# Kernel tuning notes

Hardware: AMD Instinct MI355X
Metric: run time of the kernel (lower is better)

## Reference

```python
import jax, jax.numpy as jnp
import numpy as np

X_DIM, Z_DIM, H, B, T = 257, 16, 128, 256, 512


def _p(key, shape, scale=0.05):
    return jax.random.normal(key, shape, jnp.float32) * scale


def setup_inputs() -> dict:
    key = jax.random.key(0)
    ks = jax.random.split(key, 16)
    z4 = jnp.zeros((4 * H,), jnp.float32)
    return {
        "x": jax.random.uniform(ks[0], (B, X_DIM, T), jnp.float32),
        "eps": jax.random.normal(ks[1], (T, B, Z_DIM), jnp.float32),
        # rnn_g_x: backward LSTM over x
        "Wih_gx": _p(ks[2], (4 * H, X_DIM)), "Whh_gx": _p(ks[3], (4 * H, H)),
        "bih_gx": z4, "bhh_gx": z4,
        # rnn_g_z: forward LSTM cell over sampled z
        "Wih_gz": _p(ks[4], (4 * H, Z_DIM)), "Whh_gz": _p(ks[5], (4 * H, H)),
        "bih_gz": z4, "bhh_gz": z4,
        # mlp_inference (one dense layer, tanh) + heads
        "W0": _p(ks[6], (H, 2 * H)), "b0": jnp.zeros((H,), jnp.float32),
        "Wm": _p(ks[7], (Z_DIM, H)), "bm": jnp.zeros((Z_DIM,), jnp.float32),
        "Wv": _p(ks[8], (Z_DIM, H)), "bv": jnp.zeros((Z_DIM,), jnp.float32),
        # decoder rnn_h + gen_logvar
        "Wih_h": _p(ks[9], (4 * H, Z_DIM)), "Whh_h": _p(ks[10], (4 * H, H)),
        "bih_h": z4, "bhh_h": z4,
        "Wy": _p(ks[11], (X_DIM, H)), "by": jnp.zeros((X_DIM,), jnp.float32),
    }


def _lstm(xs, Wih, Whh, b, reverse=False):
    # xs: (T, B, in); single-layer LSTM, PyTorch gate order i,f,g,o
    Bn, Hd = xs.shape[1], Whh.shape[1]

    def step(carry, x_t):
        h, c = carry
        g = x_t @ Wih.T + h @ Whh.T + b
        i, f, gg, o = jnp.split(g, 4, axis=-1)
        c = jax.nn.sigmoid(f) * c + jax.nn.sigmoid(i) * jnp.tanh(gg)
        h = jax.nn.sigmoid(o) * jnp.tanh(c)
        return (h, c), h

    init = (jnp.zeros((Bn, Hd), xs.dtype), jnp.zeros((Bn, Hd), xs.dtype))
    _, hs = jax.lax.scan(step, init, xs, reverse=reverse)
    return hs


def reference(x, eps, Wih_gx, Whh_gx, bih_gx, bhh_gx,
              Wih_gz, Whh_gz, bih_gz, bhh_gz,
              W0, b0, Wm, bm, Wv, bv,
              Wih_h, Whh_h, bih_h, bhh_h, Wy, by):
    xt = jnp.transpose(x, (2, 0, 1))  # (T, B, x_dim)
    # g_x = flip(LSTM(flip(x))) == backward-direction LSTM
    g_x = _lstm(xt, Wih_gx, Whh_gx, bih_gx + bhh_gx, reverse=True)
    bz = bih_gz + bhh_gz
    Hz = Whh_gz.shape[1]

    def inf_step(carry, inp):
        g_z, c_z = carry  # hidden of rnn_g_z BEFORE seeing current z
        gx_t, eps_t = inp
        h = jnp.tanh(jnp.concatenate([gx_t, g_z], axis=-1) @ W0.T + b0)
        mean = h @ Wm.T + bm
        logvar = h @ Wv.T + bv
        z_t = eps_t * jnp.exp(0.5 * logvar) + mean  # reparameterize
        # one LSTM-cell step of rnn_g_z on z_t (used at next timestep)
        g = z_t @ Wih_gz.T + g_z @ Whh_gz.T + bz
        i, f, gg, o = jnp.split(g, 4, axis=-1)
        c_z = jax.nn.sigmoid(f) * c_z + jax.nn.sigmoid(i) * jnp.tanh(gg)
        g_z = jax.nn.sigmoid(o) * jnp.tanh(c_z)
        return (g_z, c_z), (mean, logvar, z_t)

    Bn = xt.shape[1]
    init = (jnp.zeros((Bn, Hz), x.dtype), jnp.zeros((Bn, Hz), x.dtype))
    _, (mean, logvar, z) = jax.lax.scan(inf_step, init, (g_x, eps))
    # generation
    hdec = _lstm(z, Wih_h, Whh_h, bih_h + bhh_h)
    y = jnp.exp(hdec @ Wy.T + by)  # (T, B, x_dim)
    perm = lambda a: jnp.transpose(a, (1, 2, 0))  # -> (B, dim, T)
    return perm(y), perm(mean), perm(logvar), perm(z)
```

## Files before the change

kernel.cpp:

```cpp
#include <hip/hip_runtime.h>
#include <stdint.h>

#define T_SEQ 512
#define BATCH 256
#define HID   128
#define G4    512
#define XD    257
#define ZD    16

__device__ __forceinline__ float bf2f(uint16_t u) {
  union { uint32_t i; float f; } v; v.i = ((uint32_t)u) << 16; return v.f;
}
__device__ __forceinline__ uint16_t f2bf(float f) {
  union { float f; uint32_t i; } v; v.f = f;
  uint32_t r = v.i + 0x7fffu + ((v.i >> 16) & 1u);
  return (uint16_t)(r >> 16);
}
__device__ __forceinline__ float sigf(float x) { return 1.0f / (1.0f + __expf(-x)); }
__device__ __forceinline__ float tanhfast(float x) { return 2.0f / (1.0f + __expf(-2.0f * x)) - 1.0f; }
__device__ __forceinline__ float gate_act(float pre, bool isg) {
  float s = isg ? (-2.0f * pre) : (-pre);
  float r = 1.0f / (1.0f + __expf(s));
  return isg ? (2.0f * r - 1.0f) : r;
}

__global__ void k_prep(const float* __restrict__ Wih_gx, const float* __restrict__ Wy,
                       float* __restrict__ wT, float* __restrict__ wyT) {
  int idx = blockIdx.x * 256 + threadIdx.x;
  const int N1 = XD * G4;
  const int N2 = HID * XD;
  if (idx < N1) {
    int j = idx & (G4 - 1), d = idx >> 9;
    wT[idx] = Wih_gx[j * XD + d];
  } else if (idx < N1 + N2) {
    int i2 = idx - N1;
    int u = i2 / XD, d = i2 % XD;
    wyT[i2] = Wy[d * HID + u];
  }
}

__global__ __launch_bounds__(256) void k_proj(
    const float* __restrict__ x, const float* __restrict__ wT,
    const float* __restrict__ bih, const float* __restrict__ bhh,
    uint16_t* __restrict__ px) {
  __shared__ uint16_t xs[XD * 66];
  int tid = threadIdx.x;
  int t0 = blockIdx.x * 64, b = blockIdx.y;
  int lane = tid & 63;
  {
    int t = tid & 63, d0 = tid >> 6;
    for (int d = d0; d < XD; d += 4)
      xs[d * 66 + t] = f2bf(x[((size_t)b * XD + d) * T_SEQ + t0 + t]);
  }
  __syncthreads();
  int w = __builtin_amdgcn_readfirstlane(tid >> 6);
  for (int p = 0; p < 8; ++p) {
    int j0 = w * 128 + p * 16;
    float acc[16];
#pragma unroll
    for (int i = 0; i < 16; ++i) acc[i] = bih[j0 + i] + bhh[j0 + i];
    for (int d = 0; d < XD; ++d) {
      float xv = bf2f(xs[d * 66 + lane]);
      const float* wrow = wT + (size_t)d * G4 + j0;
#pragma unroll
      for (int i = 0; i < 16; ++i) acc[i] = fmaf(wrow[i], xv, acc[i]);
    }
    size_t base = ((size_t)(t0 + lane) * BATCH + b) * G4 + j0;
    uint32_t pk[8];
#pragma unroll
    for (int i = 0; i < 8; ++i)
      pk[i] = (uint32_t)f2bf(acc[2 * i]) | ((uint32_t)f2bf(acc[2 * i + 1]) << 16);
    uint4* dst = (uint4*)(px + base);
    dst[0] = make_uint4(pk[0], pk[1], pk[2], pk[3]);
    dst[1] = make_uint4(pk[4], pk[5], pk[6], pk[7]);
  }
}

__global__ __launch_bounds__(512, 2) void k_lstm_gx(
    const uint16_t* __restrict__ px, const float* __restrict__ Whh,
    uint16_t* __restrict__ gx) {
  __shared__ __align__(16) float hl[2][HID];
  int tid = threadIdx.x, b = blockIdx.x;
  int u = tid >> 2, g = tid & 3;
  int j = g * HID + u;
  float wr[HID];
#pragma unroll
  for (int k = 0; k < HID; ++k) wr[k] = Whh[(size_t)j * HID + k];
  if (tid < HID) hl[0][tid] = 0.0f;
  float c = 0.0f;
  int cur = 0;
  int ql = (tid & 63) & ~3;
  bool isg = (g == 2);
  uint16_t pcur = px[((size_t)(T_SEQ - 1) * BATCH + b) * G4 + j];
  __syncthreads();
  for (int t = T_SEQ - 1; t >= 0; --t) {
    int tn = t > 0 ? t - 1 : 0;
    uint16_t pnext = px[((size_t)tn * BATCH + b) * G4 + j];
    float pre = bf2f(pcur);
    const float4* h4 = (const float4*)hl[cur];
#pragma unroll
    for (int k4 = 0; k4 < HID / 4; ++k4) {
      float4 h = h4[k4];
      pre = fmaf(wr[4 * k4 + 0], h.x, pre);
      pre = fmaf(wr[4 * k4 + 1], h.y, pre);
      pre = fmaf(wr[4 * k4 + 2], h.z, pre);
      pre = fmaf(wr[4 * k4 + 3], h.w, pre);
    }
    float act = gate_act(pre, isg);
    float af = __shfl(act, ql + 1);
    float ag = __shfl(act, ql + 2);
    float ao = __shfl(act, ql + 3);
    if (g == 0) {
      c = af * c + act * ag;
      float h = ao * tanhfast(c);
      hl[cur ^ 1][u] = h;
      gx[((size_t)t * BATCH + b) * HID + u] = f2bf(h);
    }
    cur ^= 1;
    pcur = pnext;
    __syncthreads();
  }
}

__global__ __launch_bounds__(512, 2) void k_inf(
    const uint16_t* __restrict__ gx, const float* __restrict__ eps,
    const float* __restrict__ Wih_gz, const float* __restrict__ Whh_gz,
    const float* __restrict__ bih_gz, const float* __restrict__ bhh_gz,
    const float* __restrict__ W0, const float* __restrict__ b0,
    const float* __restrict__ Wm, const float* __restrict__ bm,
    const float* __restrict__ Wv, const float* __restrict__ bv,
    float* __restrict__ zbuf, float* __restrict__ out_mean,
    float* __restrict__ out_logvar, float* __restrict__ out_z) {
  __shared__ float wgzT2[ZD * 512];
  __shared__ __align__(16) float gxl[HID];
  __shared__ __align__(16) float gzl[2][HID];
  __shared__ __align__(16) float hvec[HID];
  __shared__ __align__(16) float zl[ZD];
  int tid = threadIdx.x, b = blockIdx.x;
  int u = tid >> 2, g = tid & 3;
  int j = g * HID + u;
#pragma unroll
  for (int k = 0; k < ZD; ++k) wgzT2[k * 512 + tid] = Wih_gz[(size_t)j * ZD + k];
  float wzr[HID];
#pragma unroll
  for (int k = 0; k < HID; ++k) wzr[k] = Whh_gz[(size_t)j * HID + k];
  float bzr = bih_gz[j] + bhh_gz[j];
  float w0r[64];
#pragma unroll
  for (int i = 0; i < 64; ++i) w0r[i] = W0[(size_t)u * 256 + g * 64 + i];
  float b0r = b0[u];
  int o = tid >> 5, lo = tid & 31;
  float wmr[8];
  {
    const float* Wsel = (lo < 16) ? (Wm + (size_t)o * HID + lo * 8)
                                  : (Wv + (size_t)o * HID + (lo - 16) * 8);
#pragma unroll
    for (int i = 0; i < 8; ++i) wmr[i] = Wsel[i];
  }
  float bmr = bm[o], bvr = bv[o];
  float czr = 0.0f;
  int cur = 0;
  int ql = (tid & 63) & ~3;
  bool isg = (g == 2);
  if (tid < HID) {
    gzl[0][tid] = 0.0f;
    gxl[tid] = bf2f(gx[(size_t)b * HID + tid]);
  }
  float epcur = (lo == 0) ? eps[(size_t)b * ZD + o] : 0.0f;
  __syncthreads();
  for (int t = 0; t < T_SEQ; ++t) {
    int tn = (t < T_SEQ - 1) ? t + 1 : t;
    float gxnext = (tid < HID) ? bf2f(gx[((size_t)tn * BATCH + b) * HID + tid]) : 0.0f;
    float epnext = (lo == 0) ? eps[((size_t)tn * BATCH + b) * ZD + o] : 0.0f;
    {
      const float4* src = (const float4*)((g < 2) ? (gxl + g * 64) : (gzl[cur] + (g - 2) * 64));
      float p = 0.0f;
#pragma unroll
      for (int i4 = 0; i4 < 16; ++i4) {
        float4 v = src[i4];
        p = fmaf(w0r[4 * i4 + 0], v.x, p);
        p = fmaf(w0r[4 * i4 + 1], v.y, p);
        p = fmaf(w0r[4 * i4 + 2], v.z, p);
        p = fmaf(w0r[4 * i4 + 3], v.w, p);
      }
      p += __shfl_xor(p, 1);
      p += __shfl_xor(p, 2);
      if (g == 0) hvec[u] = tanhfast(p + b0r);
    }
    __syncthreads();
    {
      int hbase = (lo & 15) * 8;
      const float4* hh = (const float4*)(hvec + hbase);
      float4 h0 = hh[0], h1 = hh[1];
      float p = wmr[0] * h0.x + wmr[1] * h0.y + wmr[2] * h0.z + wmr[3] * h0.w +
                wmr[4] * h1.x + wmr[5] * h1.y + wmr[6] * h1.z + wmr[7] * h1.w;
      p += __shfl_xor(p, 1);
      p += __shfl_xor(p, 2);
      p += __shfl_xor(p, 4);
      p += __shfl_xor(p, 8);
      float other = __shfl_xor(p, 16);
      if (lo == 0) {
        float mean = p + bmr;
        float lv = other + bvr;
        float zv = epcur * __expf(0.5f * lv) + mean;
        zl[o] = zv;
        out_mean[((size_t)b * ZD + o) * T_SEQ + t] = mean;
        out_logvar[((size_t)b * ZD + o) * T_SEQ + t] = lv;
        out_z[((size_t)b * ZD + o) * T_SEQ + t] = zv;
        zbuf[((size_t)t * BATCH + b) * ZD + o] = zv;
      }
    }
    __syncthreads();
    {
      float pre = bzr;
#pragma unroll
      for (int k = 0; k < ZD; ++k) pre = fmaf(zl[k], wgzT2[k * 512 + tid], pre);
      const float4* g4 = (const float4*)gzl[cur];
#pragma unroll
      for (int k4 = 0; k4 < HID / 4; ++k4) {
        float4 hv = g4[k4];
        pre = fmaf(wzr[4 * k4 + 0], hv.x, pre);
        pre = fmaf(wzr[4 * k4 + 1], hv.y, pre);
        pre = fmaf(wzr[4 * k4 + 2], hv.z, pre);
        pre = fmaf(wzr[4 * k4 + 3], hv.w, pre);
      }
      float act = gate_act(pre, isg);
      float af = __shfl(act, ql + 1);
      float ag = __shfl(act, ql + 2);
      float ao = __shfl(act, ql + 3);
      if (g == 0) {
        czr = af * czr + act * ag;
        gzl[cur ^ 1][u] = ao * tanhfast(czr);
      }
      if (tid < HID) gxl[tid] = gxnext;
    }
    epcur = epnext;
    cur ^= 1;
    __syncthreads();
  }
}

__global__ __launch_bounds__(512, 2) void k_dec(
    const float* __restrict__ zbuf, const float* __restrict__ Wih_h,
    const float* __restrict__ Whh_h, const float* __restrict__ bih,
    const float* __restrict__ bhh, uint16_t* __restrict__ hdec) {
  __shared__ float wihT2[ZD * 512];
  __shared__ __align__(16) float hl[2][HID];
  __shared__ float zls[2][ZD];
  int tid = threadIdx.x, b = blockIdx.x;
  int u = tid >> 2, g = tid & 3;
  int j = g * HID + u;
#pragma unroll
  for (int k = 0; k < ZD; ++k) wihT2[k * 512 + tid] = Wih_h[(size_t)j * ZD + k];
  float wr[HID];
#pragma unroll
  for (int k = 0; k < HID; ++k) wr[k] = Whh_h[(size_t)j * HID + k];
  float bz = bih[j] + bhh[j];
  if (tid < HID) hl[0][tid] = 0.0f;
  if (tid < ZD) zls[0][tid] = zbuf[(size_t)b * ZD + tid];
  float c = 0.0f;
  int cur = 0;
  int ql = (tid & 63) & ~3;
  bool isg = (g == 2);
  __syncthreads();
  for (int t = 0; t < T_SEQ; ++t) {
    int tn = (t < T_SEQ - 1) ? t + 1 : t;
    float znext = (tid < ZD) ? zbuf[((size_t)tn * BATCH + b) * ZD + tid] : 0.0f;
    float pre = bz;
#pragma unroll
    for (int k = 0; k < ZD; ++k) pre = fmaf(zls[cur][k], wihT2[k * 512 + tid], pre);
    const float4* h4 = (const float4*)hl[cur];
#pragma unroll
    for (int k4 = 0; k4 < HID / 4; ++k4) {
      float4 h = h4[k4];
      pre = fmaf(wr[4 * k4 + 0], h.x, pre);
      pre = fmaf(wr[4 * k4 + 1], h.y, pre);
      pre = fmaf(wr[4 * k4 + 2], h.z, pre);
      pre = fmaf(wr[4 * k4 + 3], h.w, pre);
    }
    float act = gate_act(pre, isg);
    float af = __shfl(act, ql + 1);
    float ag = __shfl(act, ql + 2);
    float ao = __shfl(act, ql + 3);
    if (g == 0) {
      c = af * c + act * ag;
      float h = ao * tanhfast(c);
      hl[cur ^ 1][u] = h;
      hdec[((size_t)t * BATCH + b) * HID + u] = f2bf(h);
    }
    if (tid < ZD) zls[cur ^ 1][tid] = znext;
    cur ^= 1;
    __syncthreads();
  }
}

__global__ __launch_bounds__(256) void k_y(
    const uint16_t* __restrict__ hdec, const float* __restrict__ wyT,
    const float* __restrict__ by, float* __restrict__ out_y) {
  __shared__ __align__(16) float hl[HID * 65];
  int tid = threadIdx.x;
  int t0 = blockIdx.x * 64, b = blockIdx.y;
  {
    int uu = tid & 127, tg = tid >> 7;
    for (int tt = tg; tt < 64; tt += 2)
      hl[uu * 65 + tt] = bf2f(hdec[((size_t)(t0 + tt) * BATCH + b) * HID + uu]);
  }
  __syncthreads();
  int w = __builtin_amdgcn_readfirstlane(tid >> 6);
  int lane = tid & 63;
  for (int p = 0; p < 4; ++p) {
    int d0 = w * 16 + p * 64;
    float acc[16];
#pragma unroll
    for (int i = 0; i < 16; ++i) acc[i] = by[d0 + i];
    for (int uu = 0; uu < HID; ++uu) {
      float hv = hl[uu * 65 + lane];
      const float* wrow = wyT + (size_t)uu * XD + d0;
#pragma unroll
      for (int i = 0; i < 16; ++i) acc[i] = fmaf(wrow[i], hv, acc[i]);
    }
#pragma unroll
    for (int i = 0; i < 16; ++i)
      out_y[((size_t)b * XD + d0 + i) * T_SEQ + t0 + lane] = __expf(acc[i]);
  }
  if (w == 0) {
    float acc = by[256];
    for (int uu = 0; uu < HID; ++uu)
      acc = fmaf(wyT[(size_t)uu * XD + 256], hl[uu * 65 + lane], acc);
    out_y[((size_t)b * XD + 256) * T_SEQ + t0 + lane] = __expf(acc);
  }
}

extern "C" void kernel_launch(void* const* d_in, const int* in_sizes, int n_in,
                              void* d_out, int out_size, void* d_ws, size_t ws_size,
                              hipStream_t stream) {
  const float* x      = (const float*)d_in[0];
  const float* eps    = (const float*)d_in[1];
  const float* Wih_gx = (const float*)d_in[2];
  const float* Whh_gx = (const float*)d_in[3];
  const float* bih_gx = (const float*)d_in[4];
  const float* bhh_gx = (const float*)d_in[5];
  const float* Wih_gz = (const float*)d_in[6];
  const float* Whh_gz = (const float*)d_in[7];
  const float* bih_gz = (const float*)d_in[8];
  const float* bhh_gz = (const float*)d_in[9];
  const float* W0     = (const float*)d_in[10];
  const float* b0     = (const float*)d_in[11];
  const float* Wm     = (const float*)d_in[12];
  const float* bm     = (const float*)d_in[13];
  const float* Wv     = (const float*)d_in[14];
  const float* bv     = (const float*)d_in[15];
  const float* Wih_h  = (const float*)d_in[16];
  const float* Whh_h  = (const float*)d_in[17];
  const float* bih_h  = (const float*)d_in[18];
  const float* bhh_h  = (const float*)d_in[19];
  const float* Wy     = (const float*)d_in[20];
  const float* by     = (const float*)d_in[21];

  char* ws = (char*)d_ws;
  float*    wT   = (float*)(ws + 0);
  float*    wyT  = (float*)(ws + 526336);
  uint16_t* px   = (uint16_t*)(ws + (1u << 20));
  uint16_t* gx   = (uint16_t*)(ws + 135266304);
  float*    zbuf = (float*)(ws + 168820736);
  uint16_t* hdec = (uint16_t*)(ws + 177209344);

  float* out_y      = (float*)d_out;
  float* out_mean   = out_y + (size_t)BATCH * XD * T_SEQ;
  float* out_logvar = out_mean + (size_t)BATCH * ZD * T_SEQ;
  float* out_z      = out_logvar + (size_t)BATCH * ZD * T_SEQ;

  k_prep<<<dim3(643), dim3(256), 0, stream>>>(Wih_gx, Wy, wT, wyT);
  k_proj<<<dim3(8, 256), dim3(256), 0, stream>>>(x, wT, bih_gx, bhh_gx, px);
  k_lstm_gx<<<dim3(256), dim3(512), 0, stream>>>(px, Whh_gx, gx);
  k_inf<<<dim3(256), dim3(512), 0, stream>>>(gx, eps, Wih_gz, Whh_gz, bih_gz, bhh_gz,
                                             W0, b0, Wm, bm, Wv, bv,
                                             zbuf, out_mean, out_logvar, out_z);
  k_dec<<<dim3(256), dim3(512), 0, stream>>>(zbuf, Wih_h, Whh_h, bih_h, bhh_h, hdec);
  k_y<<<dim3(8, 256), dim3(256), 0, stream>>>(hdec, wyT, by, out_y);
}
```

Before: 4.277 ms.

## Rewrite recurrent LSTM kernels with bf16 MFMA over 16-batch tiles

The three sequential kernels (backward LSTM, inference loop, decoder LSTM) now use 16x16x32 bf16 MFMA instructions instead of per-thread scalar FMA dot products. Each block handles 16 batch rows rather than one, so only 16 blocks are launched instead of 256. A new packing kernel converts the weights into MFMA fragment layout in bf16. Hidden states and z are kept in bf16 in shared memory and in the z buffer. The aim is to cut the per-step recurrence cost, in exchange for much lower GPU occupancy (16 blocks) and extra bf16 rounding in the recurrent state.

Result: slower. 4.657 ms (+8.9%).

```diff
diff --git a/kernel.cpp b/kernel.cpp
--- a/kernel.cpp
+++ b/kernel.cpp
@@ -8,6 +8,21 @@
 #define XD    257
 #define ZD    16
 
+typedef short  bf16x8 __attribute__((ext_vector_type(8)));
+typedef float  f32x4  __attribute__((ext_vector_type(4)));
+
+#define MFMA(a,b,c) __builtin_amdgcn_mfma_f32_16x16x32_bf16((a),(b),(c),0,0,0)
+
+#define OHH_GX 0
+#define OHH_GZ 8192
+#define OHH_H  16384
+#define OIH_GZ 24576
+#define OIH_H  26624
+#define OW0    28672
+#define OWM    32768
+#define OWV    33024
+#define NPACK  33280
+
 __device__ __forceinline__ float bf2f(uint16_t u) {
   union { uint32_t i; float f; } v; v.i = ((uint32_t)u) << 16; return v.f;
 }
@@ -16,7 +31,6 @@
   uint32_t r = v.i + 0x7fffu + ((v.i >> 16) & 1u);
   return (uint16_t)(r >> 16);
 }
-__device__ __forceinline__ float sigf(float x) { return 1.0f / (1.0f + __expf(-x)); }
 __device__ __forceinline__ float tanhfast(float x) { return 2.0f / (1.0f + __expf(-2.0f * x)) - 1.0f; }
 __device__ __forceinline__ float gate_act(float pre, bool isg) {
   float s = isg ? (-2.0f * pre) : (-pre);
@@ -39,6 +53,43 @@
   }
 }
 
+__global__ __launch_bounds__(256) void k_pack(
+    const float* __restrict__ Whh_gx, const float* __restrict__ Whh_gz,
+    const float* __restrict__ Whh_h,  const float* __restrict__ Wih_gz,
+    const float* __restrict__ Wih_h,  const float* __restrict__ W0,
+    const float* __restrict__ Wm,     const float* __restrict__ Wv,
+    uint4* __restrict__ out) {
+  int idx = blockIdx.x * 256 + threadIdx.x;
+  if (idx >= NPACK) return;
+  const float* W; int Kreal, KT, base; bool perm;
+  if      (idx < OHH_GZ) { W = Whh_gx; Kreal = 128; KT = 4; perm = true;  base = OHH_GX; }
+  else if (idx < OHH_H ) { W = Whh_gz; Kreal = 128; KT = 4; perm = true;  base = OHH_GZ; }
+  else if (idx < OIH_GZ) { W = Whh_h;  Kreal = 128; KT = 4; perm = true;  base = OHH_H;  }
+  else if (idx < OIH_H ) { W = Wih_gz; Kreal = 16;  KT = 1; perm = true;  base = OIH_GZ; }
+  else if (idx < OW0   ) { W = Wih_h;  Kreal = 16;  KT = 1; perm = true;  base = OIH_H;  }
+  else if (idx < OWM   ) { W = W0;     Kreal = 256; KT = 8; perm = false; base = OW0;    }
+  else if (idx < OWV   ) { W = Wm;     Kreal = 128; KT = 4; perm = false; base = OWM;    }
+  else                   { W = Wv;     Kreal = 128; KT = 4; perm = false; base = OWV;    }
+  int li = idx - base;
+  int lane = li & 63, rest = li >> 6;
+  int kt = rest % KT, tile = rest / KT;
+  int n15 = lane & 15, quad = lane >> 4;
+  int r = perm ? ((tile & 3) * 128 + (tile >> 2) * 16 + n15) : (tile * 16 + n15);
+  int k0 = kt * 32 + quad * 8;
+  uint16_t v[8];
+#pragma unroll
+  for (int j = 0; j < 8; ++j) {
+    float f = (k0 + j < Kreal) ? W[(size_t)r * Kreal + k0 + j] : 0.0f;
+    v[j] = f2bf(f);
+  }
+  uint4 o4;
+  o4.x = (uint32_t)v[0] | ((uint32_t)v[1] << 16);
+  o4.y = (uint32_t)v[2] | ((uint32_t)v[3] << 16);
+  o4.z = (uint32_t)v[4] | ((uint32_t)v[5] << 16);
+  o4.w = (uint32_t)v[6] | ((uint32_t)v[7] << 16);
+  out[idx] = o4;
+}
+
 __global__ __launch_bounds__(256) void k_proj(
     const float* __restrict__ x, const float* __restrict__ wT,
     const float* __restrict__ bih, const float* __restrict__ bhh,
@@ -66,229 +117,266 @@
       for (int i = 0; i < 16; ++i) acc[i] = fmaf(wrow[i], xv, acc[i]);
     }
     size_t base = ((size_t)(t0 + lane) * BATCH + b) * G4 + j0;
-    uint32_t pk[8];
+    uint32_t pkd[8];
 #pragma unroll
     for (int i = 0; i < 8; ++i)
-      pk[i] = (uint32_t)f2bf(acc[2 * i]) | ((uint32_t)f2bf(acc[2 * i + 1]) << 16);
+      pkd[i] = (uint32_t)f2bf(acc[2 * i]) | ((uint32_t)f2bf(acc[2 * i + 1]) << 16);
     uint4* dst = (uint4*)(px + base);
-    dst[0] = make_uint4(pk[0], pk[1], pk[2], pk[3]);
-    dst[1] = make_uint4(pk[4], pk[5], pk[6], pk[7]);
+    dst[0] = make_uint4(pkd[0], pkd[1], pkd[2], pkd[3]);
+    dst[1] = make_uint4(pkd[4], pkd[5], pkd[6], pkd[7]);
   }
 }
 
 __global__ __launch_bounds__(512, 2) void k_lstm_gx(
-    const uint16_t* __restrict__ px, const float* __restrict__ Whh,
+    const uint16_t* __restrict__ px, const uint4* __restrict__ pk,
     uint16_t* __restrict__ gx) {
-  __shared__ __align__(16) float hl[2][HID];
-  int tid = threadIdx.x, b = blockIdx.x;
-  int u = tid >> 2, g = tid & 3;
-  int j = g * HID + u;
-  float wr[HID];
-#pragma unroll
-  for (int k = 0; k < HID; ++k) wr[k] = Whh[(size_t)j * HID + k];
-  if (tid < HID) hl[0][tid] = 0.0f;
-  float c = 0.0f;
+  __shared__ uint16_t hl[2][16 * 136];
+  int tid = threadIdx.x, b0 = blockIdx.x * 16;
+  int lane = tid & 63, w = tid >> 6;
+  int n15 = lane & 15, quad = lane >> 4;
+  const bf16x8* pkb = (const bf16x8*)pk;
+  bf16x8 whh[4][4];
+#pragma unroll
+  for (int ct = 0; ct < 4; ++ct)
+#pragma unroll
+    for (int kt = 0; kt < 4; ++kt)
+      whh[ct][kt] = pkb[OHH_GX + ((4 * w + ct) * 4 + kt) * 64 + lane];
+  for (int i = tid; i < 16 * 136; i += 512) hl[0][i] = 0;
+  float c[4] = {0.f, 0.f, 0.f, 0.f};
   int cur = 0;
-  int ql = (tid & 63) & ~3;
-  bool isg = (g == 2);
-  uint16_t pcur = px[((size_t)(T_SEQ - 1) * BATCH + b) * G4 + j];
+  uint16_t pxr[4][4];
+#pragma unroll
+  for (int ct = 0; ct < 4; ++ct) {
+    int r = ct * 128 + w * 16 + n15;
+#pragma unroll
+    for (int reg = 0; reg < 4; ++reg)
+      pxr[ct][reg] = px[((size_t)(T_SEQ - 1) * BATCH + b0 + quad * 4 + reg) * G4 + r];
+  }
   __syncthreads();
   for (int t = T_SEQ - 1; t >= 0; --t) {
+    bf16x8 a[4];
+#pragma unroll
+    for (int kt = 0; kt < 4; ++kt)
+      a[kt] = *(const bf16x8*)&hl[cur][n15 * 136 + kt * 32 + quad * 8];
     int tn = t > 0 ? t - 1 : 0;
-    uint16_t pnext = px[((size_t)tn * BATCH + b) * G4 + j];
-    float pre = bf2f(pcur);
-    const float4* h4 = (const float4*)hl[cur];
-#pragma unroll
-    for (int k4 = 0; k4 < HID / 4; ++k4) {
-      float4 h = h4[k4];
-      pre = fmaf(wr[4 * k4 + 0], h.x, pre);
-      pre = fmaf(wr[4 * k4 + 1], h.y, pre);
-      pre = fmaf(wr[4 * k4 + 2], h.z, pre);
-      pre = fmaf(wr[4 * k4 + 3], h.w, pre);
-    }
-    float act = gate_act(pre, isg);
-    float af = __shfl(act, ql + 1);
-    float ag = __shfl(act, ql + 2);
-    float ao = __shfl(act, ql + 3);
-    if (g == 0) {
-      c = af * c + act * ag;
-      float h = ao * tanhfast(c);
-      hl[cur ^ 1][u] = h;
-      gx[((size_t)t * BATCH + b) * HID + u] = f2bf(h);
-    }
+    uint16_t pxn[4][4];
+#pragma unroll
+    for (int ct = 0; ct < 4; ++ct) {
+      int r = ct * 128 + w * 16 + n15;
+#pragma unroll
+      for (int reg = 0; reg < 4; ++reg)
+        pxn[ct][reg] = px[((size_t)tn * BATCH + b0 + quad * 4 + reg) * G4 + r];
+    }
+    float act[4][4];
+#pragma unroll
+    for (int ct = 0; ct < 4; ++ct) {
+      f32x4 acc = {bf2f(pxr[ct][0]), bf2f(pxr[ct][1]), bf2f(pxr[ct][2]), bf2f(pxr[ct][3])};
+#pragma unroll
+      for (int kt = 0; kt < 4; ++kt) acc = MFMA(a[kt], whh[ct][kt], acc);
+#pragma unroll
+      for (int reg = 0; reg < 4; ++reg) act[ct][reg] = gate_act(acc[reg], ct == 2);
+    }
+#pragma unroll
+    for (int reg = 0; reg < 4; ++reg) {
+      c[reg] = act[1][reg] * c[reg] + act[0][reg] * act[2][reg];
+      float h = act[3][reg] * tanhfast(c[reg]);
+      uint16_t hb = f2bf(h);
+      int m = quad * 4 + reg;
+      hl[cur ^ 1][m * 136 + w * 16 + n15] = hb;
+      gx[((size_t)t * BATCH + b0 + m) * HID + w * 16 + n15] = hb;
+    }
+#pragma unroll
+    for (int ct = 0; ct < 4; ++ct)
+#pragma unroll
+      for (int reg = 0; reg < 4; ++reg) pxr[ct][reg] = pxn[ct][reg];
     cur ^= 1;
-    pcur = pnext;
     __syncthreads();
   }
 }
 
 __global__ __launch_bounds__(512, 2) void k_inf(
     const uint16_t* __restrict__ gx, const float* __restrict__ eps,
-    const float* __restrict__ Wih_gz, const float* __restrict__ Whh_gz,
+    const uint4* __restrict__ pk,
     const float* __restrict__ bih_gz, const float* __restrict__ bhh_gz,
-    const float* __restrict__ W0, const float* __restrict__ b0,
-    const float* __restrict__ Wm, const float* __restrict__ bm,
-    const float* __restrict__ Wv, const float* __restrict__ bv,
-    float* __restrict__ zbuf, float* __restrict__ out_mean,
+    const float* __restrict__ b0, const float* __restrict__ bm,
+    const float* __restrict__ bv,
+    uint16_t* __restrict__ zbuf, float* __restrict__ out_mean,
     float* __restrict__ out_logvar, float* __restrict__ out_z) {
-  __shared__ float wgzT2[ZD * 512];
-  __shared__ __align__(16) float gxl[HID];
-  __shared__ __align__(16) float gzl[2][HID];
-  __shared__ __align__(16) float hvec[HID];
-  __shared__ __align__(16) float zl[ZD];
-  int tid = threadIdx.x, b = blockIdx.x;
-  int u = tid >> 2, g = tid & 3;
-  int j = g * HID + u;
-#pragma unroll
-  for (int k = 0; k < ZD; ++k) wgzT2[k * 512 + tid] = Wih_gz[(size_t)j * ZD + k];
-  float wzr[HID];
-#pragma unroll
-  for (int k = 0; k < HID; ++k) wzr[k] = Whh_gz[(size_t)j * HID + k];
-  float bzr = bih_gz[j] + bhh_gz[j];
-  float w0r[64];
-#pragma unroll
-  for (int i = 0; i < 64; ++i) w0r[i] = W0[(size_t)u * 256 + g * 64 + i];
-  float b0r = b0[u];
-  int o = tid >> 5, lo = tid & 31;
-  float wmr[8];
-  {
-    const float* Wsel = (lo < 16) ? (Wm + (size_t)o * HID + lo * 8)
-                                  : (Wv + (size_t)o * HID + (lo - 16) * 8);
-#pragma unroll
-    for (int i = 0; i < 8; ++i) wmr[i] = Wsel[i];
-  }
-  float bmr = bm[o], bvr = bv[o];
-  float czr = 0.0f;
+  __shared__ uint16_t gzl[2][16 * 136];
+  __shared__ uint16_t hmlp[16 * 136];
+  __shared__ uint16_t zt[16 * 40];
+  __shared__ float means[16 * 17];
+  __shared__ float lvs[16 * 17];
+  int tid = threadIdx.x, b0i = blockIdx.x * 16;
+  int lane = tid & 63, w = tid >> 6;
+  int n15 = lane & 15, quad = lane >> 4;
+  const bf16x8* pkb = (const bf16x8*)pk;
+  bf16x8 w0f[8];
+#pragma unroll
+  for (int kt = 0; kt < 8; ++kt) w0f[kt] = pkb[OW0 + (w * 8 + kt) * 64 + lane];
+  bf16x8 whz[4][4];
+#pragma unroll
+  for (int ct = 0; ct < 4; ++ct)
+#pragma unroll
+    for (int kt = 0; kt < 4; ++kt)
+      whz[ct][kt] = pkb[OHH_GZ + ((4 * w + ct) * 4 + kt) * 64 + lane];
+  float bzr[4];
+#pragma unroll
+  for (int ct = 0; ct < 4; ++ct) {
+    int r = ct * 128 + w * 16 + n15;
+    bzr[ct] = bih_gz[r] + bhh_gz[r];
+  }
+  float b0r = b0[w * 16 + n15];
+  float bmvr = (w == 0) ? bm[n15] : ((w == 1) ? bv[n15] : 0.0f);
+  for (int i = tid; i < 16 * 136; i += 512) gzl[0][i] = 0;
+  for (int i = tid; i < 16 * 40; i += 512) zt[i] = 0;
+  float c[4] = {0.f, 0.f, 0.f, 0.f};
   int cur = 0;
-  int ql = (tid & 63) & ~3;
-  bool isg = (g == 2);
-  if (tid < HID) {
-    gzl[0][tid] = 0.0f;
-    gxl[tid] = bf2f(gx[(size_t)b * HID + tid]);
-  }
-  float epcur = (lo == 0) ? eps[(size_t)b * ZD + o] : 0.0f;
+  int zm = tid >> 4, zo = tid & 15;
+  float epr = (tid < 256) ? eps[(size_t)(b0i + zm) * ZD + zo] : 0.0f;
+  bf16x8 gxf[4];
+#pragma unroll
+  for (int kt = 0; kt < 4; ++kt)
+    gxf[kt] = *(const bf16x8*)(gx + ((size_t)(b0i + n15)) * HID + kt * 32 + quad * 8);
   __syncthreads();
   for (int t = 0; t < T_SEQ; ++t) {
+    bf16x8 gzf[4];
+#pragma unroll
+    for (int kt = 0; kt < 4; ++kt)
+      gzf[kt] = *(const bf16x8*)&gzl[cur][n15 * 136 + kt * 32 + quad * 8];
+    f32x4 hb = {b0r, b0r, b0r, b0r};
+#pragma unroll
+    for (int kt = 0; kt < 4; ++kt) hb = MFMA(gxf[kt], w0f[kt], hb);
+#pragma unroll
+    for (int kt = 0; kt < 4; ++kt) hb = MFMA(gzf[kt], w0f[4 + kt], hb);
     int tn = (t < T_SEQ - 1) ? t + 1 : t;
-    float gxnext = (tid < HID) ? bf2f(gx[((size_t)tn * BATCH + b) * HID + tid]) : 0.0f;
-    float epnext = (lo == 0) ? eps[((size_t)tn * BATCH + b) * ZD + o] : 0.0f;
-    {
-      const float4* src = (const float4*)((g < 2) ? (gxl + g * 64) : (gzl[cur] + (g - 2) * 64));
-      float p = 0.0f;
-#pragma unroll
-      for (int i4 = 0; i4 < 16; ++i4) {
-        float4 v = src[i4];
-        p = fmaf(w0r[4 * i4 + 0], v.x, p);
-        p = fmaf(w0r[4 * i4 + 1], v.y, p);
-        p = fmaf(w0r[4 * i4 + 2], v.z, p);
-        p = fmaf(w0r[4 * i4 + 3], v.w, p);
+    bf16x8 gxn[4];
+#pragma unroll
+    for (int kt = 0; kt < 4; ++kt)
+      gxn[kt] = *(const bf16x8*)(gx + ((size_t)tn * BATCH + b0i + n15) * HID + kt * 32 + quad * 8);
+    float epn = (tid < 256) ? eps[((size_t)tn * BATCH + b0i + zm) * ZD + zo] : 0.0f;
+#pragma unroll
+    for (int reg = 0; reg < 4; ++reg)
+      hmlp[(quad * 4 + reg) * 136 + w * 16 + n15] = f2bf(tanhfast(hb[reg]));
+    __syncthreads();
+    if (w < 2) {
+      f32x4 mac = {bmvr, bmvr, bmvr, bmvr};
+#pragma unroll
+      for (int kt = 0; kt < 4; ++kt) {
+        bf16x8 ha = *(const bf16x8*)&hmlp[n15 * 136 + kt * 32 + quad * 8];
+        bf16x8 wf = pkb[(w == 0 ? OWM : OWV) + kt * 64 + lane];
+        mac = MFMA(ha, wf, mac);
       }
-      p += __shfl_xor(p, 1);
-      p += __shfl_xor(p, 2);
-      if (g == 0) hvec[u] = tanhfast(p + b0r);
-    }
-    __syncthreads();
-    {
-      int hbase = (lo & 15) * 8;
-      const float4* hh = (const float4*)(hvec + hbase);
-      float4 h0 = hh[0], h1 = hh[1];
-      float p = wmr[0] * h0.x + wmr[1] * h0.y + wmr[2] * h0.z + wmr[3] * h0.w +
-                wmr[4] * h1.x + wmr[5] * h1.y + wmr[6] * h1.z + wmr[7] * h1.w;
-      p += __shfl_xor(p, 1);
-      p += __shfl_xor(p, 2);
-      p += __shfl_xor(p, 4);
-      p += __shfl_xor(p, 8);
-      float other = __shfl_xor(p, 16);
-      if (lo == 0) {
-        float mean = p + bmr;
-        float lv = other + bvr;
-        float zv = epcur * __expf(0.5f * lv) + mean;
-        zl[o] = zv;
-        out_mean[((size_t)b * ZD + o) * T_SEQ + t] = mean;
-        out_logvar[((size_t)b * ZD + o) * T_SEQ + t] = lv;
-        out_z[((size_t)b * ZD + o) * T_SEQ + t] = zv;
-        zbuf[((size_t)t * BATCH + b) * ZD + o] = zv;
+#pragma unroll
+      for (int reg = 0; reg < 4; ++reg) {
+        int m = quad * 4 + reg;
+        if (w == 0) {
+          means[m * 17 + n15] = mac[reg];
+          out_mean[((size_t)(b0i + m) * ZD + n15) * T_SEQ + t] = mac[reg];
+        } else {
+          lvs[m * 17 + n15] = mac[reg];
+          out_logvar[((size_t)(b0i + m) * ZD + n15) * T_SEQ + t] = mac[reg];
+        }
       }
     }
     __syncthreads();
-    {
-      float pre = bzr;
-#pragma unroll
-      for (int k = 0; k < ZD; ++k) pre = fmaf(zl[k], wgzT2[k * 512 + tid], pre);
-      const float4* g4 = (const float4*)gzl[cur];
-#pragma unroll
-      for (int k4 = 0; k4 < HID / 4; ++k4) {
-        float4 hv = g4[k4];
-        pre = fmaf(wzr[4 * k4 + 0], hv.x, pre);
-        pre = fmaf(wzr[4 * k4 + 1], hv.y, pre);
-        pre = fmaf(wzr[4 * k4 + 2], hv.z, pre);
-        pre = fmaf(wzr[4 * k4 + 3], hv.w, pre);
-      }
-      float act = gate_act(pre, isg);
-      float af = __shfl(act, ql + 1);
-      float ag = __shfl(act, ql + 2);
-      float ao = __shfl(act, ql + 3);
-      if (g == 0) {
-        czr = af * czr + act * ag;
-        gzl[cur ^ 1][u] = ao * tanhfast(czr);
-      }
-      if (tid < HID) gxl[tid] = gxnext;
-    }
-    epcur = epnext;
+    if (tid < 256) {
+      float mean = means[zm * 17 + zo], lv = lvs[zm * 17 + zo];
+      float zv = epr * __expf(0.5f * lv) + mean;
+      uint16_t zb = f2bf(zv);
+      zt[zm * 40 + zo] = zb;
+      zbuf[((size_t)t * BATCH + b0i + zm) * ZD + zo] = zb;
+      out_z[((size_t)(b0i + zm) * ZD + zo) * T_SEQ + t] = zv;
+    }
+    __syncthreads();
+    bf16x8 za = *(const bf16x8*)&zt[n15 * 40 + quad * 8];
+    float act[4][4];
+#pragma unroll
+    for (int ct = 0; ct < 4; ++ct) {
+      f32x4 ga = {bzr[ct], bzr[ct], bzr[ct], bzr[ct]};
+      bf16x8 wih = pkb[OIH_GZ + (4 * w + ct) * 64 + lane];
+      ga = MFMA(za, wih, ga);
+#pragma unroll
+      for (int kt = 0; kt < 4; ++kt) ga = MFMA(gzf[kt], whz[ct][kt], ga);
+#pragma unroll
+      for (int reg = 0; reg < 4; ++reg) act[ct][reg] = gate_act(ga[reg], ct == 2);
+    }
+#pragma unroll
+    for (int reg = 0; reg < 4; ++reg) {
+      c[reg] = act[1][reg] * c[reg] + act[0][reg] * act[2][reg];
+      float h = act[3][reg] * tanhfast(c[reg]);
+      gzl[cur ^ 1][(quad * 4 + reg) * 136 + w * 16 + n15] = f2bf(h);
+    }
+#pragma unroll
+    for (int kt = 0; kt < 4; ++kt) gxf[kt] = gxn[kt];
+    epr = epn;
     cur ^= 1;
     __syncthreads();
   }
 }
 
 __global__ __launch_bounds__(512, 2) void k_dec(
-    const float* __restrict__ zbuf, const float* __restrict__ Wih_h,
-    const float* __restrict__ Whh_h, const float* __restrict__ bih,
-    const float* __restrict__ bhh, uint16_t* __restrict__ hdec) {
-  __shared__ float wihT2[ZD * 512];
-  __shared__ __align__(16) float hl[2][HID];
-  __shared__ float zls[2][ZD];
-  int tid = threadIdx.x, b = blockIdx.x;
-  int u = tid >> 2, g = tid & 3;
-  int j = g * HID + u;
-#pragma unroll
-  for (int k = 0; k < ZD; ++k) wihT2[k * 512 + tid] = Wih_h[(size_t)j * ZD + k];
-  float wr[HID];
-#pragma unroll
-  for (int k = 0; k < HID; ++k) wr[k] = Whh_h[(size_t)j * HID + k];
-  float bz = bih[j] + bhh[j];
-  if (tid < HID) hl[0][tid] = 0.0f;
-  if (tid < ZD) zls[0][tid] = zbuf[(size_t)b * ZD + tid];
-  float c = 0.0f;
+    const uint16_t* __restrict__ zbuf, const uint4* __restrict__ pk,
+    const float* __restrict__ bih, const float* __restrict__ bhh,
+    uint16_t* __restrict__ hdec) {
+  __shared__ uint16_t gzl[2][16 * 136];
+  __shared__ uint16_t zt[16 * 40];
+  int tid = threadIdx.x, b0 = blockIdx.x * 16;
+  int lane = tid & 63, w = tid >> 6;
+  int n15 = lane & 15, quad = lane >> 4;
+  const bf16x8* pkb = (const bf16x8*)pk;
+  bf16x8 whh[4][4];
+#pragma unroll
+  for (int ct = 0; ct < 4; ++ct)
+#pragma unroll
+    for (int kt = 0; kt < 4; ++kt)
+      whh[ct][kt] = pkb[OHH_H + ((4 * w + ct) * 4 + kt) * 64 + lane];
+  bf16x8 wih[4];
+#pragma unroll
+  for (int ct = 0; ct < 4; ++ct) wih[ct] = pkb[OIH_H + (4 * w + ct) * 64 + lane];
+  float bzr[4];
+#pragma unroll
+  for (int ct = 0; ct < 4; ++ct) {
+    int r = ct * 128 + w * 16 + n15;
+    bzr[ct] = bih[r] + bhh[r];
+  }
+  for (int i = tid; i < 16 * 136; i += 512) gzl[0][i] = 0;
+  for (int i = tid; i < 16 * 40; i += 512) zt[i] = 0;
+  float c[4] = {0.f, 0.f, 0.f, 0.f};
   int cur = 0;
-  int ql = (tid & 63) & ~3;
-  bool isg = (g == 2);
+  int zm = tid >> 4, zo = tid & 15;
+  uint16_t zr = (tid < 256) ? zbuf[(size_t)(b0 + zm) * ZD + zo] : (uint16_t)0;
   __syncthreads();
   for (int t = 0; t < T_SEQ; ++t) {
+    if (tid < 256) zt[zm * 40 + zo] = zr;
+    __syncthreads();
+    bf16x8 za = *(const bf16x8*)&zt[n15 * 40 + quad * 8];
+    bf16x8 gzf[4];
+#pragma unroll
+    for (int kt = 0; kt < 4; ++kt)
+      gzf[kt] = *(const bf16x8*)&gzl[cur][n15 * 136 + kt * 32 + quad * 8];
     int tn = (t < T_SEQ - 1) ? t + 1 : t;
-    float znext = (tid < ZD) ? zbuf[((size_t)tn * BATCH + b) * ZD + tid] : 0.0f;
-    float pre = bz;
-#pragma unroll
-    for (int k = 0; k < ZD; ++k) pre = fmaf(zls[cur][k], wihT2[k * 512 + tid], pre);
-    const float4* h4 = (const float4*)hl[cur];
-#pragma unroll
-    for (int k4 = 0; k4 < HID / 4; ++k4) {
-      float4 h = h4[k4];
-      pre = fmaf(wr[4 * k4 + 0], h.x, pre);
-      pre = fmaf(wr[4 * k4 + 1], h.y, pre);
-      pre = fmaf(wr[4 * k4 + 2], h.z, pre);
-      pre = fmaf(wr[4 * k4 + 3], h.w, pre);
-    }
-    float act = gate_act(pre, isg);
-    float af = __shfl(act, ql + 1);
-    float ag = __shfl(act, ql + 2);
-    float ao = __shfl(act, ql + 3);
-    if (g == 0) {
-      c = af * c + act * ag;
-      float h = ao * tanhfast(c);
-      hl[cur ^ 1][u] = h;
-      hdec[((size_t)t * BATCH + b) * HID + u] = f2bf(h);
-    }
-    if (tid < ZD) zls[cur ^ 1][tid] = znext;
+    uint16_t zn = (tid < 256) ? zbuf[((size_t)tn * BATCH + b0 + zm) * ZD + zo] : (uint16_t)0;
+    float act[4][4];
+#pragma unroll
+    for (int ct = 0; ct < 4; ++ct) {
+      f32x4 ga = {bzr[ct], bzr[ct], bzr[ct], bzr[ct]};
+      ga = MFMA(za, wih[ct], ga);
+#pragma unroll
+      for (int kt = 0; kt < 4; ++kt) ga = MFMA(gzf[kt], whh[ct][kt], ga);
+#pragma unroll
+      for (int reg = 0; reg < 4; ++reg) act[ct][reg] = gate_act(ga[reg], ct == 2);
+    }
+#pragma unroll
+    for (int reg = 0; reg < 4; ++reg) {
+      c[reg] = act[1][reg] * c[reg] + act[0][reg] * act[2][reg];
+      float h = act[3][reg] * tanhfast(c[reg]);
+      uint16_t hb = f2bf(h);
+      int m = quad * 4 + reg;
+      gzl[cur ^ 1][m * 136 + w * 16 + n15] = hb;
+      hdec[((size_t)t * BATCH + b0 + m) * HID + w * 16 + n15] = hb;
+    }
+    zr = zn;
     cur ^= 1;
     __syncthreads();
   }
@@ -360,10 +448,11 @@
   char* ws = (char*)d_ws;
   float*    wT   = (float*)(ws + 0);
   float*    wyT  = (float*)(ws + 526336);
-  uint16_t* px   = (uint16_t*)(ws + (1u << 20));
-  uint16_t* gx   = (uint16_t*)(ws + 135266304);
-  float*    zbuf = (float*)(ws + 168820736);
-  uint16_t* hdec = (uint16_t*)(ws + 177209344);
+  uint4*    pkw  = (uint4*)(ws + 1048576);
+  uint16_t* px   = (uint16_t*)(ws + 2097152);
+  uint16_t* gx   = (uint16_t*)(ws + 136314880);
+  uint16_t* zbuf = (uint16_t*)(ws + 169869312);
+  uint16_t* hdec = (uint16_t*)(ws + 174063616);
 
   float* out_y      = (float*)d_out;
   float* out_mean   = out_y + (size_t)BATCH * XD * T_SEQ;
@@ -371,11 +460,12 @@
   float* out_z      = out_logvar + (size_t)BATCH * ZD * T_SEQ;
 
   k_prep<<<dim3(643), dim3(256), 0, stream>>>(Wih_gx, Wy, wT, wyT);
+  k_pack<<<dim3((NPACK + 255) / 256), dim3(256), 0, stream>>>(
+      Whh_gx, Whh_gz, Whh_h, Wih_gz, Wih_h, W0, Wm, Wv, pkw);
   k_proj<<<dim3(8, 256), dim3(256), 0, stream>>>(x, wT, bih_gx, bhh_gx, px);
-  k_lstm_gx<<<dim3(256), dim3(512), 0, stream>>>(px, Whh_gx, gx);
-  k_inf<<<dim3(256), dim3(512), 0, stream>>>(gx, eps, Wih_gz, Whh_gz, bih_gz, bhh_gz,
-                                             W0, b0, Wm, bm, Wv, bv,
-                                             zbuf, out_mean, out_logvar, out_z);
-  k_dec<<<dim3(256), dim3(512), 0, stream>>>(zbuf, Wih_h, Whh_h, bih_h, bhh_h, hdec);
+  k_lstm_gx<<<dim3(16), dim3(512), 0, stream>>>(px, pkw, gx);
+  k_inf<<<dim3(16), dim3(512), 0, stream>>>(gx, eps, pkw, bih_gz, bhh_gz,
+                                            b0, bm, bv, zbuf, out_mean, out_logvar, out_z);
+  k_dec<<<dim3(16), dim3(512), 0, stream>>>(zbuf, pkw, bih_h, bhh_h, hdec);
   k_y<<<dim3(8, 256), dim3(256), 0, stream>>>(hdec, wyT, by, out_y);
 }
```
